# Kernel tuning notes

Hardware: AMD Instinct MI355X
Metric: run time of the kernel (lower is better)

Reference implementation:

```python
import jax, jax.numpy as jnp
import numpy as np

H = 8          # n_channels
NEIGHBORS = 5


def setup_inputs() -> dict:
    key = jax.random.key(0)
    k1, k2 = jax.random.split(key)
    B, N, C = 8, 1024, 256
    x = jax.random.normal(k1, (B, N, C), dtype=jnp.float32)
    # torch Linear weight: [out_features, in_features] = [2*H*C, C]
    W_qk = jax.random.normal(k2, (2 * H * C, C), dtype=jnp.float32) * (C ** -0.5)
    return {"x": x, "W_qk": W_qk}


def _forward(x, W_qk):
    B, N, C = x.shape
    scale = C ** -0.5
    qk = (x @ W_qk.T).reshape(B, N, 2, H, C).transpose(2, 0, 3, 1, 4)
    q, k = qk[0], qk[1]                              # [B,H,N,C]
    attn = jax.nn.softmax(jnp.einsum('bhnc,bhmc->bhnm', q, k) * scale, axis=-1)

    # clip(): top-k on detached channel-summed attention
    sum_edge = jnp.sum(jax.lax.stop_gradient(attn), axis=1)   # [B,N,N]
    _, index = jax.lax.top_k(sum_edge, NEIGHBORS)             # [B,N,NEIGHBORS]
    # Faithful to source: every mask row gets 1 at the union of ALL rows'
    # top-k indices (inner loop iterates over all rows of `inds`), plus eye(N).
    flat_idx = index.reshape(B, N * NEIGHBORS)                # [B, N*nb]
    col_mask = jnp.zeros((B, N), dtype=attn.dtype).at[
        jnp.arange(B)[:, None], flat_idx].set(1.0)            # [B,N]
    mask = jnp.maximum(jnp.eye(N, dtype=attn.dtype)[None], col_mask[:, None, :])  # [B,N,N]

    new_edge = mask[:, None] * attn                           # [B,H,N,N]

    # norm_edge(): row norm, then col norm, then row @ col^T
    norm_row = new_edge / (jnp.sum(new_edge, axis=-1, keepdims=True) + 1e-16)
    norm_col = norm_row / (jnp.sum(norm_row, axis=-2, keepdims=True) + 1e-16)
    return jnp.einsum('bhnm,bhkm->bhnk', norm_row, norm_col)  # [B,H,N,N]


def reference(x, W_qk):
    return _forward(x, W_qk)
```

## Files before the change

### kernel.cpp

```cpp
#include <hip/hip_runtime.h>
#include <hip/hip_bf16.h>
#include <cstdint>
#include <cstddef>

#define BB 8
#define HH 8
#define NN 1024
#define CC 256
#define OUTCH 4096

typedef __attribute__((ext_vector_type(8))) __bf16 bf16x8;
typedef __attribute__((ext_vector_type(4))) __bf16 bf16x4;
typedef __attribute__((ext_vector_type(4))) float f32x4;

__device__ inline void async16(const void* g, void* l)
{
  __builtin_amdgcn_global_load_lds(
      reinterpret_cast<const __attribute__((address_space(1))) unsigned int*>(
          reinterpret_cast<uintptr_t>(g)),
      reinterpret_cast<__attribute__((address_space(3))) unsigned int*>(
          reinterpret_cast<uintptr_t>(l)),
      16, 0, 0);
}

__device__ inline float waveMax(float v) {
#pragma unroll
  for (int o = 32; o > 0; o >>= 1) v = fmaxf(v, __shfl_xor(v, o, 64));
  return v;
}
__device__ inline float waveSum(float v) {
#pragma unroll
  for (int o = 32; o > 0; o >>= 1) v += __shfl_xor(v, o, 64);
  return v;
}

__global__ __launch_bounds__(256) void split_kernel(const float* __restrict__ in,
                                                    __bf16* __restrict__ hi,
                                                    __bf16* __restrict__ lo, int n4)
{
  const int i = blockIdx.x * 256 + threadIdx.x;
  if (i >= n4) return;
  const float4 v = ((const float4*)in)[i];
  bf16x4 h, l;
  h.x = (__bf16)v.x; l.x = (__bf16)(v.x - (float)h.x);
  h.y = (__bf16)v.y; l.y = (__bf16)(v.y - (float)h.y);
  h.z = (__bf16)v.z; l.z = (__bf16)(v.z - (float)h.z);
  h.w = (__bf16)v.w; l.w = (__bf16)(v.w - (float)h.w);
  ((bf16x4*)hi)[i] = h;
  ((bf16x4*)lo)[i] = l;
}

__global__ __launch_bounds__(256) void xw_mfma_kernel(
    const __bf16* __restrict__ Ah, const __bf16* __restrict__ Al,
    const __bf16* __restrict__ Bh, const __bf16* __restrict__ Bl,
    __bf16* __restrict__ Chi, __bf16* __restrict__ Clo)
{
  __shared__ __bf16 AsH[128 * 32], AsL[128 * 32], BsH[128 * 32], BsL[128 * 32];

  const int tid = threadIdx.x, lane = tid & 63, wid = tid >> 6;
  const int wr = wid >> 1, wc = wid & 1;
  const int bM = blockIdx.y * 128, bN = blockIdx.x * 128;

  const int srow = wid * 16 + (lane >> 2);
  const int scol = (lane & 3) * 8;
  const __bf16* gAh = Ah + (size_t)(bM + srow) * CC + scol;
  const __bf16* gAl = Al + (size_t)(bM + srow) * CC + scol;
  const __bf16* gBh = Bh + (size_t)(bN + srow) * CC + scol;
  const __bf16* gBl = Bl + (size_t)(bN + srow) * CC + scol;
  char* lAh = (char*)AsH + wid * 16 * 64;
  char* lAl = (char*)AsL + wid * 16 * 64;
  char* lBh = (char*)BsH + wid * 16 * 64;
  char* lBl = (char*)BsL + wid * 16 * 64;

  f32x4 acc[4][4];
  const f32x4 z = {0.f, 0.f, 0.f, 0.f};
#pragma unroll
  for (int m = 0; m < 4; ++m)
#pragma unroll
    for (int n = 0; n < 4; ++n) acc[m][n] = z;

  for (int k0 = 0; k0 < CC; k0 += 32) {
    async16(gAh + k0, lAh); async16(gAh + k0 + 64 * CC, lAh + 64 * 64);
    async16(gAl + k0, lAl); async16(gAl + k0 + 64 * CC, lAl + 64 * 64);
    async16(gBh + k0, lBh); async16(gBh + k0 + 64 * CC, lBh + 64 * 64);
    async16(gBl + k0, lBl); async16(gBl + k0 + 64 * CC, lBl + 64 * 64);
    __syncthreads();

    bf16x8 ah[4], al[4], bh_[4], bl_[4];
    const int fb = (lane & 15) * 64 + (lane >> 4) * 16;
#pragma unroll
    for (int m = 0; m < 4; ++m) {
      ah[m] = *(const bf16x8*)((const char*)AsH + (wr * 64 + m * 16) * 64 + fb);
      al[m] = *(const bf16x8*)((const char*)AsL + (wr * 64 + m * 16) * 64 + fb);
    }
#pragma unroll
    for (int n = 0; n < 4; ++n) {
      bh_[n] = *(const bf16x8*)((const char*)BsH + (wc * 64 + n * 16) * 64 + fb);
      bl_[n] = *(const bf16x8*)((const char*)BsL + (wc * 64 + n * 16) * 64 + fb);
    }
#pragma unroll
    for (int m = 0; m < 4; ++m)
#pragma unroll
      for (int n = 0; n < 4; ++n) {
        acc[m][n] = __builtin_amdgcn_mfma_f32_16x16x32_bf16(al[m], bh_[n], acc[m][n], 0, 0, 0);
        acc[m][n] = __builtin_amdgcn_mfma_f32_16x16x32_bf16(ah[m], bl_[n], acc[m][n], 0, 0, 0);
        acc[m][n] = __builtin_amdgcn_mfma_f32_16x16x32_bf16(ah[m], bh_[n], acc[m][n], 0, 0, 0);
      }
    __syncthreads();
  }

  const int fr = lane & 15;
  const int fq = lane >> 4;
#pragma unroll
  for (int m = 0; m < 4; ++m) {
    const int row0 = bM + wr * 64 + m * 16 + fq * 4;
#pragma unroll
    for (int n = 0; n < 4; ++n) {
      const int col = bN + wc * 64 + n * 16 + fr;
#pragma unroll
      for (int r = 0; r < 4; ++r) {
        const float v = acc[m][n][r];
        const __bf16 h = (__bf16)v;
        const __bf16 l = (__bf16)(v - (float)h);
        Chi[(size_t)(row0 + r) * OUTCH + col] = h;
        Clo[(size_t)(row0 + r) * OUTCH + col] = l;
      }
    }
  }
}

__global__ __launch_bounds__(256) void qkt_mfma_kernel(
    const __bf16* __restrict__ Qh, const __bf16* __restrict__ Ql,
    float* __restrict__ outall)
{
  const int f = blockIdx.x;
  const int xcd = f & 7;
  const int g = f >> 3;
  const int bh = xcd + 8 * (g >> 6);
  const int tile = g & 63;
  const int b = bh >> 3, h = bh & 7;
  const size_t qoff = (size_t)b * NN * OUTCH + (size_t)h * CC;
  const size_t koff = qoff + 2048;
  float* C = outall + ((size_t)bh << 20);

  __shared__ __bf16 AsH[128 * 32], AsL[128 * 32], BsH[128 * 32], BsL[128 * 32];

  const int tid = threadIdx.x, lane = tid & 63, wid = tid >> 6;
  const int wr = wid >> 1, wc = wid & 1;
  const int bM = (tile >> 3) * 128, bN = (tile & 7) * 128;

  const int srow = wid * 16 + (lane >> 2);
  const int scol = (lane & 3) * 8;
  const __bf16* gAh = Qh + qoff + (size_t)(bM + srow) * OUTCH + scol;
  const __bf16* gAl = Ql + qoff + (size_t)(bM + srow) * OUTCH + scol;
  const __bf16* gBh = Qh + koff + (size_t)(bN + srow) * OUTCH + scol;
  const __bf16* gBl = Ql + koff + (size_t)(bN + srow) * OUTCH + scol;
  char* lAh = (char*)AsH + wid * 16 * 64;
  char* lAl = (char*)AsL + wid * 16 * 64;
  char* lBh = (char*)BsH + wid * 16 * 64;
  char* lBl = (char*)BsL + wid * 16 * 64;

  f32x4 acc[4][4];
  const f32x4 z = {0.f, 0.f, 0.f, 0.f};
#pragma unroll
  for (int m = 0; m < 4; ++m)
#pragma unroll
    for (int n = 0; n < 4; ++n) acc[m][n] = z;

  for (int k0 = 0; k0 < CC; k0 += 32) {
    async16(gAh + k0, lAh); async16(gAh + k0 + (size_t)64 * OUTCH, lAh + 64 * 64);
    async16(gAl + k0, lAl); async16(gAl + k0 + (size_t)64 * OUTCH, lAl + 64 * 64);
    async16(gBh + k0, lBh); async16(gBh + k0 + (size_t)64 * OUTCH, lBh + 64 * 64);
    async16(gBl + k0, lBl); async16(gBl + k0 + (size_t)64 * OUTCH, lBl + 64 * 64);
    __syncthreads();

    bf16x8 ah[4], al[4], bh_[4], bl_[4];
    const int fb = (lane & 15) * 64 + (lane >> 4) * 16;
#pragma unroll
    for (int m = 0; m < 4; ++m) {
      ah[m] = *(const bf16x8*)((const char*)AsH + (wr * 64 + m * 16) * 64 + fb);
      al[m] = *(const bf16x8*)((const char*)AsL + (wr * 64 + m * 16) * 64 + fb);
    }
#pragma unroll
    for (int n = 0; n < 4; ++n) {
      bh_[n] = *(const bf16x8*)((const char*)BsH + (wc * 64 + n * 16) * 64 + fb);
      bl_[n] = *(const bf16x8*)((const char*)BsL + (wc * 64 + n * 16) * 64 + fb);
    }
#pragma unroll
    for (int m = 0; m < 4; ++m)
#pragma unroll
      for (int n = 0; n < 4; ++n) {
        acc[m][n] = __builtin_amdgcn_mfma_f32_16x16x32_bf16(al[m], bh_[n], acc[m][n], 0, 0, 0);
        acc[m][n] = __builtin_amdgcn_mfma_f32_16x16x32_bf16(ah[m], bl_[n], acc[m][n], 0, 0, 0);
        acc[m][n] = __builtin_amdgcn_mfma_f32_16x16x32_bf16(ah[m], bh_[n], acc[m][n], 0, 0, 0);
      }
    __syncthreads();
  }

  const int fr = lane & 15;
  const int fq = lane >> 4;
#pragma unroll
  for (int m = 0; m < 4; ++m) {
    const int row0 = bM + wr * 64 + m * 16 + fq * 4;
#pragma unroll
    for (int n = 0; n < 4; ++n) {
      const int col = bN + wc * 64 + n * 16 + fr;
#pragma unroll
      for (int r = 0; r < 4; ++r)
        C[(size_t)(row0 + r) * NN + col] = acc[m][n][r] * 0.0625f;
    }
  }
}

__global__ __launch_bounds__(256) void softmax_se_kernel(const float* __restrict__ logits,
                                                         __bf16* __restrict__ attnb,
                                                         float* __restrict__ se)
{
  const int bn = blockIdx.x;
  const int b = bn >> 10;
  const int n = bn & 1023;
  const int t = threadIdx.x;
  const int lane = t & 63, wv = t >> 6;
  __shared__ float wred[4];
  float4 acc = make_float4(0.f, 0.f, 0.f, 0.f);

#pragma unroll 1
  for (int h = 0; h < HH; ++h) {
    const size_t rowbase = (((size_t)(b * HH + h) << 10) + n) << 10;
    const float* ar = logits + rowbase;
    __bf16* arb = attnb + rowbase;
    float4 x = *(const float4*)(ar + (t << 2));
    float mx = waveMax(fmaxf(fmaxf(x.x, x.y), fmaxf(x.z, x.w)));
    if (lane == 0) wred[wv] = mx;
    __syncthreads();
    const float M = fmaxf(fmaxf(wred[0], wred[1]), fmaxf(wred[2], wred[3]));
    __syncthreads();

    float e0 = expf(x.x - M), e1 = expf(x.y - M), e2 = expf(x.z - M), e3 = expf(x.w - M);
    float s = waveSum(e0 + e1 + e2 + e3);
    if (lane == 0) wred[wv] = s;
    __syncthreads();
    const float inv = 1.0f / (wred[0] + wred[1] + wred[2] + wred[3]);

    const float o0 = e0 * inv, o1 = e1 * inv, o2 = e2 * inv, o3 = e3 * inv;
    bf16x4 ob; ob.x = (__bf16)o0; ob.y = (__bf16)o1; ob.z = (__bf16)o2; ob.w = (__bf16)o3;
    *(bf16x4*)(arb + (t << 2)) = ob;
    acc.x += o0; acc.y += o1; acc.z += o2; acc.w += o3;
    __syncthreads();
  }
  *(float4*)(se + (size_t)bn * NN + (t << 2)) = acc;
}

__global__ __launch_bounds__(256) void topk_kernel(const float* __restrict__ se,
                                                   float* __restrict__ colmask)
{
  const int bn = blockIdx.x;
  const int b = bn >> 10;
  const int t = threadIdx.x;
  __shared__ float vals[NN];
  __shared__ unsigned long long red[256];
  const float* rowp = se + (size_t)bn * NN;
  for (int i = t; i < NN; i += 256) vals[i] = rowp[i];
  __syncthreads();

  for (int it = 0; it < 5; ++it) {
    unsigned long long best = 0ull;
    for (int i = t; i < NN; i += 256) {
      const float v = vals[i];
      if (v >= 0.f) {
        unsigned long long key =
            ((unsigned long long)__float_as_uint(v) << 32) | (unsigned)(NN - 1 - i);
        if (key > best) best = key;
      }
    }
    red[t] = best; __syncthreads();
    for (int s = 128; s > 0; s >>= 1) {
      if (t < s) red[t] = red[t] > red[t+s] ? red[t] : red[t+s];
      __syncthreads();
    }
    if (t == 0) {
      const int idx = NN - 1 - (int)(red[0] & 0xFFFFFFFFull);
      colmask[b * NN + idx] = 1.0f;
      vals[idx] = -1.0f;
    }
    __syncthreads();
  }
}

__global__ __launch_bounds__(256) void cs_rs_kernel(const __bf16* __restrict__ attnb,
                                                    const float* __restrict__ colmask,
                                                    float* __restrict__ inv_rs,
                                                    float* __restrict__ part)
{
  const int bh = blockIdx.y;
  const int b = bh >> 3;
  const int chunk = blockIdx.x;
  const int t = threadIdx.x, lane = t & 63, wv = t >> 6;
  const __bf16* ab = attnb + ((size_t)bh << 20);
  const float* cm = colmask + b * NN;
  const int c0 = lane * 16;

  float cmv[16];
#pragma unroll
  for (int q = 0; q < 4; ++q) {
    const float4 c4 = *(const float4*)(cm + c0 + q * 4);
    cmv[q*4+0] = c4.x; cmv[q*4+1] = c4.y; cmv[q*4+2] = c4.z; cmv[q*4+3] = c4.w;
  }

  float a[16];
#pragma unroll
  for (int j = 0; j < 16; ++j) a[j] = 0.f;

  const int nbase = chunk * 64 + wv * 16;
#pragma unroll 1
  for (int r = 0; r < 16; ++r) {
    const int n = nbase + r;
    const __bf16* rowp = ab + ((size_t)n << 10) + c0;
    const bf16x8 v0 = *(const bf16x8*)(rowp);
    const bf16x8 v1 = *(const bf16x8*)(rowp + 8);
    float e[16];
    float rsum = 0.f;
#pragma unroll
    for (int j = 0; j < 8; ++j) {
      const float val = ((cmv[j] != 0.f) || (c0 + j == n)) ? (float)v0[j] : 0.f;
      e[j] = val; rsum += val;
    }
#pragma unroll
    for (int j = 0; j < 8; ++j) {
      const float val = ((cmv[8+j] != 0.f) || (c0 + 8 + j == n)) ? (float)v1[j] : 0.f;
      e[8+j] = val; rsum += val;
    }
    rsum = waveSum(rsum);
    const float ir = 1.0f / (rsum + 1e-16f);
    if (lane == 0) inv_rs[bh * NN + n] = ir;
#pragma unroll
    for (int j = 0; j < 16; ++j) a[j] += e[j] * ir;
  }

  __shared__ float l[4][NN];
#pragma unroll
  for (int j = 0; j < 16; ++j) l[wv][c0 + j] = a[j];
  __syncthreads();
  const int m0 = t << 2;
  float4 o;
  o.x = l[0][m0+0] + l[1][m0+0] + l[2][m0+0] + l[3][m0+0];
  o.y = l[0][m0+1] + l[1][m0+1] + l[2][m0+1] + l[3][m0+1];
  o.z = l[0][m0+2] + l[1][m0+2] + l[2][m0+2] + l[3][m0+2];
  o.w = l[0][m0+3] + l[1][m0+3] + l[2][m0+3] + l[3][m0+3];
  *(float4*)(part + (((size_t)chunk * (BB*HH) + bh) << 10) + m0) = o;
}

__global__ __launch_bounds__(256) void cs_fin_kernel(const float* __restrict__ part,
                                                     float* __restrict__ isc)
{
  const int bh = blockIdx.x;
  const int m0 = threadIdx.x << 2;
  float a0 = 0.f, a1 = 0.f, a2 = 0.f, a3 = 0.f;
#pragma unroll
  for (int c = 0; c < 16; ++c) {
    const float4 p = *(const float4*)(part + (((size_t)c * (BB*HH) + bh) << 10) + m0);
    a0 += p.x; a1 += p.y; a2 += p.z; a3 += p.w;
  }
  float4 o;
  o.x = 1.0f / sqrtf(a0 + 1e-16f);
  o.y = 1.0f / sqrtf(a1 + 1e-16f);
  o.z = 1.0f / sqrtf(a2 + 1e-16f);
  o.w = 1.0f / sqrtf(a3 + 1e-16f);
  *(float4*)(isc + ((size_t)bh << 10) + m0) = o;
}

__global__ __launch_bounds__(256) void g_kernel(const __bf16* __restrict__ attnb,
                                                const float* __restrict__ colmask,
                                                const float* __restrict__ inv_rs,
                                                const float* __restrict__ isc,
                                                __bf16* __restrict__ Gb)
{
  const size_t idx = ((size_t)blockIdx.x * 256 + threadIdx.x) << 2;
  const size_t row = idx >> 10;
  const int m = (int)(idx & 1023);
  const int n = (int)(row & 1023);
  const int bh = (int)(row >> 10);
  const int b = bh >> 3;
  const bf16x4 vb = *(const bf16x4*)(attnb + idx);
  const float4 c = *(const float4*)(colmask + b * NN + m);
  const float4 s = *(const float4*)(isc + ((size_t)bh << 10) + m);
  const float ir = inv_rs[row];
  bf16x4 o;
  o.x = (__bf16)((((c.x != 0.f) || (m + 0 == n)) ? (float)vb.x : 0.f) * ir * s.x);
  o.y = (__bf16)((((c.y != 0.f) || (m + 1 == n)) ? (float)vb.y : 0.f) * ir * s.y);
  o.z = (__bf16)((((c.z != 0.f) || (m + 2 == n)) ? (float)vb.z : 0.f) * ir * s.z);
  o.w = (__bf16)((((c.w != 0.f) || (m + 3 == n)) ? (float)vb.w : 0.f) * ir * s.w);
  *(bf16x4*)(Gb + idx) = o;
}

__global__ __launch_bounds__(256) void ggt_mfma_kernel(const __bf16* __restrict__ Gball,
                                                       float* __restrict__ outall)
{
  const int f = blockIdx.x;
  const int xcd = f & 7;
  const int g = f >> 3;
  const int bh = xcd + 8 * (g / 36);
  int tt = g % 36;

  const __bf16* A = Gball + ((size_t)bh << 20);
  float* C = outall + ((size_t)bh << 20);

  int ti = 0;
#pragma unroll
  for (int r = 0; r < 8; ++r) {
    const int len = 8 - r;
    if (tt < len) { ti = r; break; }
    tt -= len;
  }
  const int tj = ti + tt;

  __shared__ __bf16 As[128 * 32];
  __shared__ __bf16 Bs[128 * 32];

  const int tid  = threadIdx.x;
  const int lane = tid & 63;
  const int wid  = tid >> 6;
  const int wr   = wid >> 1;
  const int wc   = wid & 1;
  const int bM   = ti * 128;
  const int bN   = tj * 128;

  const int srow = wid * 16 + (lane >> 2);
  const int scol = (lane & 3) * 8;
  const __bf16* gA = A + (size_t)(bM + srow) * NN + scol;
  const __bf16* gB = A + (size_t)(bN + srow) * NN + scol;
  char* lA = (char*)As + wid * 16 * 64;
  char* lB = (char*)Bs + wid * 16 * 64;

  f32x4 acc[4][4];
  const f32x4 z = {0.f, 0.f, 0.f, 0.f};
#pragma unroll
  for (int m = 0; m < 4; ++m)
#pragma unroll
    for (int n = 0; n < 4; ++n) acc[m][n] = z;

  for (int k0 = 0; k0 < NN; k0 += 32) {
    async16(gA + k0,           lA);
    async16(gA + k0 + 64 * NN, lA + 64 * 64);
    async16(gB + k0,           lB);
    async16(gB + k0 + 64 * NN, lB + 64 * 64);
    __syncthreads();

    bf16x8 a[4], b[4];
    const int fb = (lane & 15) * 64 + (lane >> 4) * 16;
#pragma unroll
    for (int m = 0; m < 4; ++m)
      a[m] = *(const bf16x8*)((const char*)As + (wr * 64 + m * 16) * 64 + fb);
#pragma unroll
    for (int n = 0; n < 4; ++n)
      b[n] = *(const bf16x8*)((const char*)Bs + (wc * 64 + n * 16) * 64 + fb);
#pragma unroll
    for (int m = 0; m < 4; ++m)
#pragma unroll
      for (int n = 0; n < 4; ++n)
        acc[m][n] = __builtin_amdgcn_mfma_f32_16x16x32_bf16(a[m], b[n], acc[m][n], 0, 0, 0);
    __syncthreads();
  }

  const int fr = lane & 15;
  const int fq = lane >> 4;
#pragma unroll
  for (int m = 0; m < 4; ++m) {
    const int row0 = bM + wr * 64 + m * 16 + fq * 4;
#pragma unroll
    for (int n = 0; n < 4; ++n) {
      const int col = bN + wc * 64 + n * 16 + fr;
#pragma unroll
      for (int r = 0; r < 4; ++r)
        C[(size_t)(row0 + r) * NN + col] = acc[m][n][r];
    }
  }
  if (ti != tj) {
#pragma unroll
    for (int m = 0; m < 4; ++m) {
      const int colT = bM + wr * 64 + m * 16 + fq * 4;
#pragma unroll
      for (int n = 0; n < 4; ++n) {
        const int rowT = bN + wc * 64 + n * 16 + fr;
        *(f32x4*)(C + (size_t)rowT * NN + colT) = acc[m][n];
      }
    }
  }
}

extern "C" void kernel_launch(void* const* d_in, const int* in_sizes, int n_in,
                              void* d_out, int out_size, void* d_ws, size_t ws_size,
                              hipStream_t stream)
{
  const float* x = (const float*)d_in[0];
  const float* W = (const float*)d_in[1];
  float* logits = (float*)d_out;
  char* ws = (char*)d_ws;

  __bf16* qk_hi = (__bf16*)(ws + ((size_t)0   << 20));
  __bf16* qk_lo = (__bf16*)(ws + ((size_t)64  << 20));
  __bf16* attnb = (__bf16*)(ws + ((size_t)0   << 20));
  __bf16* x_hi  = (__bf16*)(ws + ((size_t)128 << 20));
  __bf16* x_lo  = (__bf16*)(ws + ((size_t)132 << 20));
  __bf16* W_hi  = (__bf16*)(ws + ((size_t)136 << 20));
  __bf16* W_lo  = (__bf16*)(ws + ((size_t)138 << 20));
  float*  se    = (float*)(ws + ((size_t)144 << 20));
  float*  cmask = (float*)(ws + ((size_t)176 << 20));
  float*  irs   = (float*)(ws + ((size_t)177 << 20));
  float*  isc   = (float*)(ws + ((size_t)178 << 20));
  float*  csp   = (float*)(ws + ((size_t)180 << 20));
  __bf16* Gb    = (__bf16*)(ws + ((size_t)192 << 20));

  hipLaunchKernelGGL(split_kernel, dim3((BB*NN*CC/4 + 255)/256), dim3(256), 0, stream,
                     x, x_hi, x_lo, BB*NN*CC/4);
  hipLaunchKernelGGL(split_kernel, dim3((OUTCH*CC/4 + 255)/256), dim3(256), 0, stream,
                     W, W_hi, W_lo, OUTCH*CC/4);

  hipLaunchKernelGGL(xw_mfma_kernel, dim3(OUTCH/128, (BB*NN)/128, 1), dim3(256), 0, stream,
                     x_hi, x_lo, W_hi, W_lo, qk_hi, qk_lo);

  hipLaunchKernelGGL(qkt_mfma_kernel, dim3(64 * 64), dim3(256), 0, stream,
                     qk_hi, qk_lo, logits);

  hipLaunchKernelGGL(softmax_se_kernel, dim3(BB*NN), dim3(256), 0, stream,
                     logits, attnb, se);

  hipMemsetAsync(cmask, 0, (size_t)BB * NN * 4, stream);
  hipLaunchKernelGGL(topk_kernel, dim3(BB*NN), dim3(256), 0, stream, se, cmask);

  hipLaunchKernelGGL(cs_rs_kernel, dim3(16, BB*HH), dim3(256), 0, stream,
                     attnb, cmask, irs, csp);
  hipLaunchKernelGGL(cs_fin_kernel, dim3(BB*HH), dim3(256), 0, stream, csp, isc);

  hipLaunchKernelGGL(g_kernel, dim3((BB*HH*NN*(long long)NN) / 4 / 256), dim3(256), 0, stream,
                     attnb, cmask, irs, isc, Gb);

  hipLaunchKernelGGL(ggt_mfma_kernel, dim3(36 * 64), dim3(256), 0, stream,
                     Gb, logits);

  (void)in_sizes; (void)n_in; (void)out_size; (void)ws_size;
}
```

Baseline: 561.3 us.

## Double-buffer LDS in the symmetric G GEMM and merge split launches

The final symmetric GEMM kernel now uses two LDS buffers, so the next K-slice is prefetched with async global-to-LDS loads while MFMAs run on the current one. A partial vmcnt wait and raw barriers replace full __syncthreads. The two fp32-to-bf16 hi/lo split kernels are also merged into one launch covering both x and W. LDS use doubles in the GEMM, which may lower occupancy, and the hand-placed waitcnt ordering must stay correct.

```diff
diff --git a/kernel.cpp b/kernel.cpp
--- a/kernel.cpp
+++ b/kernel.cpp
@@ -34,20 +34,24 @@
   return v;
 }
 
-__global__ __launch_bounds__(256) void split_kernel(const float* __restrict__ in,
-                                                    __bf16* __restrict__ hi,
-                                                    __bf16* __restrict__ lo, int n4)
-{
-  const int i = blockIdx.x * 256 + threadIdx.x;
-  if (i >= n4) return;
-  const float4 v = ((const float4*)in)[i];
+__global__ __launch_bounds__(256) void split2_kernel(
+    const float* __restrict__ x, const float* __restrict__ W,
+    __bf16* __restrict__ xh, __bf16* __restrict__ xl,
+    __bf16* __restrict__ Wh, __bf16* __restrict__ Wl)
+{
+  const int NX = BB * NN * CC / 4;
+  int i = blockIdx.x * 256 + threadIdx.x;
+  const float* in; __bf16* ph; __bf16* pl; int j;
+  if (i < NX) { in = x; ph = xh; pl = xl; j = i; }
+  else        { in = W; ph = Wh; pl = Wl; j = i - NX; }
+  const float4 v = ((const float4*)in)[j];
   bf16x4 h, l;
   h.x = (__bf16)v.x; l.x = (__bf16)(v.x - (float)h.x);
   h.y = (__bf16)v.y; l.y = (__bf16)(v.y - (float)h.y);
   h.z = (__bf16)v.z; l.z = (__bf16)(v.z - (float)h.z);
   h.w = (__bf16)v.w; l.w = (__bf16)(v.w - (float)h.w);
-  ((bf16x4*)hi)[i] = h;
-  ((bf16x4*)lo)[i] = l;
+  ((bf16x4*)ph)[j] = h;
+  ((bf16x4*)pl)[j] = l;
 }
 
 __global__ __launch_bounds__(256) void xw_mfma_kernel(
@@ -414,8 +418,8 @@
   }
   const int tj = ti + tt;
 
-  __shared__ __bf16 As[128 * 32];
-  __shared__ __bf16 Bs[128 * 32];
+  __shared__ __bf16 As[2][128 * 32];
+  __shared__ __bf16 Bs[2][128 * 32];
 
   const int tid  = threadIdx.x;
   const int lane = tid & 63;
@@ -429,8 +433,7 @@
   const int scol = (lane & 3) * 8;
   const __bf16* gA = A + (size_t)(bM + srow) * NN + scol;
   const __bf16* gB = A + (size_t)(bN + srow) * NN + scol;
-  char* lA = (char*)As + wid * 16 * 64;
-  char* lB = (char*)Bs + wid * 16 * 64;
+  const int lofs = wid * 16 * 64;
 
   f32x4 acc[4][4];
   const f32x4 z = {0.f, 0.f, 0.f, 0.f};
@@ -439,27 +442,58 @@
 #pragma unroll
     for (int n = 0; n < 4; ++n) acc[m][n] = z;
 
-  for (int k0 = 0; k0 < NN; k0 += 32) {
-    async16(gA + k0,           lA);
-    async16(gA + k0 + 64 * NN, lA + 64 * 64);
-    async16(gB + k0,           lB);
-    async16(gB + k0 + 64 * NN, lB + 64 * 64);
-    __syncthreads();
+  const int fb = (lane & 15) * 64 + (lane >> 4) * 16;
+
+  async16(gA,           (char*)As[0] + lofs);
+  async16(gA + 64 * NN, (char*)As[0] + lofs + 64 * 64);
+  async16(gB,           (char*)Bs[0] + lofs);
+  async16(gB + 64 * NN, (char*)Bs[0] + lofs + 64 * 64);
+
+  int cur = 0;
+#pragma unroll 1
+  for (int k0 = 0; k0 < NN - 32; k0 += 32) {
+    const int nxt = cur ^ 1;
+    async16(gA + k0 + 32,           (char*)As[nxt] + lofs);
+    async16(gA + k0 + 32 + 64 * NN, (char*)As[nxt] + lofs + 64 * 64);
+    async16(gB + k0 + 32,           (char*)Bs[nxt] + lofs);
+    async16(gB + k0 + 32 + 64 * NN, (char*)Bs[nxt] + lofs + 64 * 64);
+    asm volatile("s_waitcnt vmcnt(4)" ::: "memory");
+    __builtin_amdgcn_s_barrier();
+    __builtin_amdgcn_sched_barrier(0);
 
     bf16x8 a[4], b[4];
-    const int fb = (lane & 15) * 64 + (lane >> 4) * 16;
 #pragma unroll
     for (int m = 0; m < 4; ++m)
-      a[m] = *(const bf16x8*)((const char*)As + (wr * 64 + m * 16) * 64 + fb);
+      a[m] = *(const bf16x8*)((const char*)As[cur] + (wr * 64 + m * 16) * 64 + fb);
 #pragma unroll
     for (int n = 0; n < 4; ++n)
-      b[n] = *(const bf16x8*)((const char*)Bs + (wc * 64 + n * 16) * 64 + fb);
+      b[n] = *(const bf16x8*)((const char*)Bs[cur] + (wc * 64 + n * 16) * 64 + fb);
 #pragma unroll
     for (int m = 0; m < 4; ++m)
 #pragma unroll
       for (int n = 0; n < 4; ++n)
         acc[m][n] = __builtin_amdgcn_mfma_f32_16x16x32_bf16(a[m], b[n], acc[m][n], 0, 0, 0);
-    __syncthreads();
+    __builtin_amdgcn_s_barrier();
+    __builtin_amdgcn_sched_barrier(0);
+    cur ^= 1;
+  }
+
+  asm volatile("s_waitcnt vmcnt(0)" ::: "memory");
+  __builtin_amdgcn_s_barrier();
+  __builtin_amdgcn_sched_barrier(0);
+  {
+    bf16x8 a[4], b[4];
+#pragma unroll
+    for (int m = 0; m < 4; ++m)
+      a[m] = *(const bf16x8*)((const char*)As[cur] + (wr * 64 + m * 16) * 64 + fb);
+#pragma unroll
+    for (int n = 0; n < 4; ++n)
+      b[n] = *(const bf16x8*)((const char*)Bs[cur] + (wc * 64 + n * 16) * 64 + fb);
+#pragma unroll
+    for (int m = 0; m < 4; ++m)
+#pragma unroll
+      for (int n = 0; n < 4; ++n)
+        acc[m][n] = __builtin_amdgcn_mfma_f32_16x16x32_bf16(a[m], b[n], acc[m][n], 0, 0, 0);
   }
 
   const int fr = lane & 15;
@@ -511,10 +545,8 @@
   float*  csp   = (float*)(ws + ((size_t)180 << 20));
   __bf16* Gb    = (__bf16*)(ws + ((size_t)192 << 20));
 
-  hipLaunchKernelGGL(split_kernel, dim3((BB*NN*CC/4 + 255)/256), dim3(256), 0, stream,
-                     x, x_hi, x_lo, BB*NN*CC/4);
-  hipLaunchKernelGGL(split_kernel, dim3((OUTCH*CC/4 + 255)/256), dim3(256), 0, stream,
-                     W, W_hi, W_lo, OUTCH*CC/4);
+  hipLaunchKernelGGL(split2_kernel, dim3((BB*NN*CC + OUTCH*CC) / 4 / 256), dim3(256), 0, stream,
+                     x, W, x_hi, x_lo, W_hi, W_lo);
 
   hipLaunchKernelGGL(xw_mfma_kernel, dim3(OUTCH/128, (BB*NN)/128, 1), dim3(256), 0, stream,
                      x_hi, x_lo, W_hi, W_lo, qk_hi, qk_lo);
```

After: 553.0 us. No clear change (-1.5%).
